# Kernel tuning notes

Hardware: AMD Instinct MI355X
Metric: run time of the kernel (lower is better)

## Reference

```python
import jax, jax.numpy as jnp
import numpy as np

B, S, H, D, R = 2, 2048, 16, 128, 16
HID = H * D
ROPE_BASE = 10000.0


def _rotate_half(x):
    x1, x2 = x[..., : D // 2], x[..., D // 2:]
    return jnp.concatenate((-x2, x1), axis=-1)


def _sin_cos(position_ids):
    # full-dim RoPE (rope_fraction == 1)
    inv_freq = 1.0 / (ROPE_BASE ** (jnp.arange(0, D, 2, dtype=jnp.float32) / D))  # [D/2]
    freqs = position_ids.astype(jnp.float32)[..., None] * inv_freq  # [B,S,D/2]
    emb = jnp.concatenate((freqs, freqs), axis=-1)  # [B,S,D]
    # add head axis -> [B,1,S,D]
    return jnp.sin(emb)[:, None], jnp.cos(emb)[:, None]


def setup_inputs() -> dict:
    key = jax.random.key(0)
    ks = jax.random.split(key, 6)
    q = jax.random.normal(ks[0], (B, S, HID), dtype=jnp.float32)
    k = jax.random.normal(ks[1], (B, S, HID), dtype=jnp.float32)
    v = jax.random.normal(ks[2], (B, S, HID), dtype=jnp.float32)
    position_ids = jnp.tile(jnp.arange(S, dtype=jnp.int64)[None], (B, 1))
    causal = jnp.tril(jnp.ones((S, S), dtype=bool))
    attention_mask = jnp.where(causal, 0.0, -1e9).astype(jnp.float32)
    attention_mask = jnp.broadcast_to(attention_mask[None, None], (B, 1, S, S))
    k_registers = jax.random.normal(ks[3], (1, H, R, D), dtype=jnp.float32)
    v_registers = jax.random.normal(ks[4], (1, H, R, D), dtype=jnp.float32)
    return {
        "query_states": q,
        "key_states": k,
        "value_states": v,
        "position_ids": position_ids,
        "attention_mask": attention_mask,
        "k_registers": k_registers,
        "v_registers": v_registers,
    }


def reference(query_states, key_states, value_states, position_ids,
              attention_mask, k_registers, v_registers):
    bsz, q_len, _ = query_states.shape
    # [B,S,H*D] -> [B,H,S,D]
    q = query_states.reshape(bsz, q_len, H, D).transpose(0, 2, 1, 3)
    k = key_states.reshape(bsz, -1, H, D).transpose(0, 2, 1, 3)
    v = value_states.reshape(bsz, -1, H, D).transpose(0, 2, 1, 3)

    sin, cos = _sin_cos(position_ids)
    q = q * cos + _rotate_half(q) * sin
    k = k * cos + _rotate_half(k) * sin

    # concat learned register K/V tokens along kv-length
    k = jnp.concatenate((k, jnp.broadcast_to(k_registers, (bsz, H, R, D))), axis=2)
    v = jnp.concatenate((v, jnp.broadcast_to(v_registers, (bsz, H, R, D))), axis=2)
    mask = jnp.concatenate(
        (attention_mask,
         jnp.zeros(attention_mask.shape[:-1] + (R,), dtype=attention_mask.dtype)),
        axis=-1)

    scale = 1.0 / np.sqrt(D).astype(np.float32)
    scores = jnp.einsum('bhqd,bhkd->bhqk', q, k * scale) + mask  # [B,H,S,S+R]
    probs = jax.nn.softmax(scores.astype(jnp.float32), axis=-1).astype(q.dtype)
    out = jnp.einsum('bhqk,bhkd->bhqd', probs, v)
    return out.transpose(0, 2, 1, 3).reshape(bsz, q_len, H * D)
```

## Files before the change

### kernel.cpp

```cpp
#include <hip/hip_runtime.h>

#define S_LEN 2048
#define HID   2048
#define NH    16
#define HD    128
#define NREG  16
#define KPAD  2112
#define NBH   32

typedef float f32x4 __attribute__((ext_vector_type(4)));
typedef short s16x8 __attribute__((ext_vector_type(8)));

__device__ __forceinline__ unsigned short f2bf(float f) {
    union { float f; unsigned int u; } x; x.f = f;
    return (unsigned short)((x.u + 0x7FFFu + ((x.u >> 16) & 1u)) >> 16);
}
__device__ __forceinline__ unsigned short f2bf_t(float f) {
    union { float f; unsigned int u; } x; x.f = f;
    return (unsigned short)(x.u >> 16);
}
__device__ __forceinline__ void gl_lds16(const unsigned short* g, unsigned short* l) {
    __builtin_amdgcn_global_load_lds((const __attribute__((address_space(1))) void*)g,
                                     (__attribute__((address_space(3))) void*)l, 16, 0, 0);
}
__device__ __forceinline__ void barrier_lgkm() {
    asm volatile("s_waitcnt lgkmcnt(0)\n\ts_barrier" ::: "memory");
}

__global__ void prepass_kernel(const float* __restrict__ k, const float* __restrict__ v,
                               const int* __restrict__ pos,
                               const float* __restrict__ kreg, const float* __restrict__ vreg,
                               unsigned short* __restrict__ Kb, unsigned short* __restrict__ Vt) {
    __shared__ unsigned short T[64][136];
    int bid = blockIdx.x, tid = threadIdx.x;

    if (bid < 4096) {
        int i  = bid * 256 + tid;
        int d4 = (i & 15) << 2;
        int h  = (i >> 4) & 15;
        int s  = (i >> 8) & 2047;
        int b  = i >> 19;
        float p = (float)pos[b * S_LEN + s];
        const float* kp = k + (size_t)(b * S_LEN + s) * HID + h * HD + d4;
        float4 k1 = *(const float4*)kp, k2 = *(const float4*)(kp + 64);
        const float* k1f = (const float*)&k1; const float* k2f = (const float*)&k2;
        unsigned short ok1[4], ok2[4];
        #pragma unroll
        for (int j = 0; j < 4; ++j) {
            float inv = exp2f((float)(d4 + j) * -0.20762050593046014f);
            float rev = p * inv * 0.15915494309189535f;
            rev -= rintf(rev);
            float a2 = rev * 6.283185307179586f;
            float sn = __sinf(a2), cs = __cosf(a2);
            ok1[j] = f2bf(k1f[j] * cs - k2f[j] * sn);
            ok2[j] = f2bf(k2f[j] * cs + k1f[j] * sn);
        }
        uint2 a;
        size_t ko = (size_t)((b * NH + h) * KPAD + s) * HD + d4;
        a.x = (unsigned)ok1[0] | ((unsigned)ok1[1] << 16);
        a.y = (unsigned)ok1[2] | ((unsigned)ok1[3] << 16);
        *(uint2*)(Kb + ko) = a;
        a.x = (unsigned)ok2[0] | ((unsigned)ok2[1] << 16);
        a.y = (unsigned)ok2[2] | ((unsigned)ok2[3] << 16);
        *(uint2*)(Kb + ko + 64) = a;
    } else if (bid < 5120) {
        int vb = bid - 4096;
        int tt = tid;
        int bh = vb >> 5, st = vb & 31;
        int b  = bh >> 4, h = bh & 15;
        {
            int key = tt >> 2, c = tt & 3;
            const float* src = v + (size_t)(b * S_LEN + st * 64 + key) * HID + h * HD;
            #pragma unroll
            for (int i = 0; i < 4; ++i) {
                int d0 = c * 32 + i * 8;
                float4 aa = *(const float4*)(src + d0);
                float4 bb = *(const float4*)(src + d0 + 4);
                unsigned short tmp[8] = { f2bf(aa.x), f2bf(aa.y), f2bf(aa.z), f2bf(aa.w),
                                          f2bf(bb.x), f2bf(bb.y), f2bf(bb.z), f2bf(bb.w) };
                *(uint4*)(&T[key][d0]) = *(const uint4*)tmp;
            }
        }
        __syncthreads();
        {
            int d = tt >> 1, half = tt & 1;
            unsigned short buf[32];
            #pragma unroll
            for (int i = 0; i < 32; ++i) buf[i] = T[half * 32 + i][d];
            uint4* dst = (uint4*)(Vt + ((size_t)(bh * HD + d)) * KPAD + st * 64 + half * 32);
            const uint4* bp = (const uint4*)buf;
            #pragma unroll
            for (int i = 0; i < 4; ++i) dst[i] = bp[i];
        }
    } else {
        int i = (bid - 5120) * 256 + tid;
        {
            int d = i & 127, r = (i >> 7) & 63, h = (i >> 13) & 15, b = i >> 17;
            float x = (r < NREG) ? kreg[(h * NREG + r) * HD + d] : 0.0f;
            Kb[((size_t)((b * NH + h) * KPAD + 2048 + r)) * HD + d] = f2bf(x);
        }
        {
            int r = i & 63, d = (i >> 6) & 127, h = (i >> 13) & 15, b = i >> 17;
            float x = (r < NREG) ? vreg[(h * NREG + r) * HD + d] : 0.0f;
            Vt[((size_t)((b * NH + h) * HD + d)) * KPAD + 2048 + r] = f2bf(x);
        }
    }
}

__global__ __launch_bounds__(256, 2)
void attn_kernel(const float* __restrict__ q, const int* __restrict__ pos,
                 const unsigned short* __restrict__ Kb,
                 const unsigned short* __restrict__ Vt, float* __restrict__ out) {
    __shared__ unsigned short Klds[64 * 128];
    __shared__ unsigned short Vtl[2 * 128 * 64];
    __shared__ unsigned short Plds[4 * 16 * 72];

    int idx = blockIdx.x;
    int bh  = idx & 31;
    int j5  = idx >> 5;
    int t   = (idx < 256) ? (15 - 2 * j5) : (2 * (j5 - 8));
    int b = bh >> 4, h = bh & 15;
    int tid = threadIdx.x, w = tid >> 6, lane = tid & 63;
    int quad = lane >> 4, k15 = lane & 15;
    int s0q = t * 128;

    const unsigned short* kg[4]; unsigned short* klp[4];
    const unsigned short* vg[4]; unsigned short* vlp[4];
    {
        int krow = 16 * w + (lane >> 4);
        #pragma unroll
        for (int j = 0; j < 4; ++j) {
            int key = krow + 4 * j;
            kg[j]  = Kb + ((size_t)bh * KPAD + key) * HD + (((lane & 15) ^ (key & 15)) << 3);
            klp[j] = Klds + (16 * w + 4 * j) * HD;
        }
        int drow = 32 * w + (lane >> 3);
        int vsw  = ((lane & 7) ^ (lane >> 3)) << 3;
        #pragma unroll
        for (int j = 0; j < 4; ++j) {
            vg[j]  = Vt + ((size_t)bh * HD + drow + 8 * j) * KPAD + vsw;
            vlp[j] = Vtl + (32 * w + 8 * j) * 64;
        }
    }
    auto stageK = [&](int kbase) {
        size_t ko = (size_t)kbase * HD;
        #pragma unroll
        for (int j = 0; j < 4; ++j) gl_lds16(kg[j] + ko, klp[j]);
    };
    auto stageV = [&](int kbase, int buf) {
        #pragma unroll
        for (int j = 0; j < 4; ++j) gl_lds16(vg[j] + kbase, vlp[j] + buf * 8192);
    };

    s16x8 qa[2][4];
    #pragma unroll
    for (int mt = 0; mt < 2; ++mt) {
        int row = s0q + w * 32 + mt * 16 + k15;
        float p = (float)pos[b * S_LEN + row];
        const float* qp = q + (size_t)(b * S_LEN + row) * HID + h * HD + quad * 8;
        #pragma unroll
        for (int kc = 0; kc < 2; ++kc) {
            float4 xa = *(const float4*)(qp + kc * 32);
            float4 xb = *(const float4*)(qp + kc * 32 + 4);
            float4 ya = *(const float4*)(qp + kc * 32 + 64);
            float4 yb = *(const float4*)(qp + kc * 32 + 68);
            float x1[8] = {xa.x, xa.y, xa.z, xa.w, xb.x, xb.y, xb.z, xb.w};
            float x2[8] = {ya.x, ya.y, ya.z, ya.w, yb.x, yb.y, yb.z, yb.w};
            unsigned short lo[8], hi[8];
            #pragma unroll
            for (int j = 0; j < 8; ++j) {
                int dh = kc * 32 + quad * 8 + j;
                float inv = exp2f((float)dh * -0.20762050593046014f);
                float rev = p * inv * 0.15915494309189535f;
                rev -= rintf(rev);
                float a2 = rev * 6.283185307179586f;
                float sn = __sinf(a2), cs = __cosf(a2);
                const float scale = 0.08838834764831845f;
                lo[j] = f2bf((x1[j] * cs - x2[j] * sn) * scale);
                hi[j] = f2bf((x2[j] * cs + x1[j] * sn) * scale);
            }
            qa[mt][kc]     = *(const s16x8*)lo;
            qa[mt][kc + 2] = *(const s16x8*)hi;
        }
    }

    f32x4 oacc[2][8];
    float lsum[2][4];
    #pragma unroll
    for (int mt = 0; mt < 2; ++mt) {
        #pragma unroll
        for (int nc = 0; nc < 8; ++nc) oacc[mt][nc] = (f32x4){0.f, 0.f, 0.f, 0.f};
        #pragma unroll
        for (int r = 0; r < 4; ++r) lsum[mt][r] = 0.f;
    }

    auto qk = [&](f32x4* sc, int mt, int mode) {
        #pragma unroll
        for (int nc = 0; nc < 4; ++nc) {
            sc[nc] = (f32x4){0.f, 0.f, 0.f, 0.f};
            if (mode == 2 && nc > 0) continue;
            #pragma unroll
            for (int kc = 0; kc < 4; ++kc) {
                const s16x8 bf = *(const s16x8*)(Klds + (nc * 16 + k15) * HD +
                                                 (((4 * kc + quad) ^ k15) << 3));
                sc[nc] = __builtin_amdgcn_mfma_f32_16x16x32_bf16(qa[mt][kc], bf, sc[nc], 0, 0, 0);
            }
        }
    };
    auto smax = [&](const f32x4* sc, int mt, int mode, int coff) {
        int rowb = w * 32 + mt * 16 + quad * 4;
        #pragma unroll
        for (int r = 0; r < 4; ++r) {
            float p[4];
            #pragma unroll
            for (int nc = 0; nc < 4; ++nc) {
                if (mode == 2 && nc > 0) { p[nc] = 0.f; continue; }
                float e = __expf(sc[nc][r]);
                bool valid = (mode != 1) || (coff + nc * 16 + k15 <= rowb + r);
                p[nc] = valid ? e : 0.f;
            }
            lsum[mt][r] += (p[0] + p[1]) + (p[2] + p[3]);
            int prow = w * (16 * 72) + (quad * 4 + r) * 72 + k15;
            Plds[prow]      = f2bf_t(p[0]);
            Plds[prow + 16] = f2bf_t(p[1]);
            Plds[prow + 32] = f2bf_t(p[2]);
            Plds[prow + 48] = f2bf_t(p[3]);
        }
    };
    auto pv = [&](int mt, int mode, const unsigned short* Vc) {
        #pragma unroll
        for (int kc = 0; kc < 2; ++kc) {
            if (mode == 2 && kc > 0) continue;
            const s16x8 pf = *(const s16x8*)(Plds + w * (16 * 72) + k15 * 72 +
                                             kc * 32 + quad * 8);
            #pragma unroll
            for (int nc = 0; nc < 8; ++nc) {
                const s16x8 vf = *(const s16x8*)(Vc + (nc * 16 + k15) * 64 +
                                                 (((4 * kc + quad) ^ (k15 & 7)) << 3));
                oacc[mt][nc] = __builtin_amdgcn_mfma_f32_16x16x32_bf16(pf, vf, oacc[mt][nc], 0, 0, 0);
            }
        }
    };

    stageK(0);
    stageV(0, 0);
    __syncthreads();

    int cur = 0;
    int NT  = 2 * t + 3;
    #pragma unroll 1
    for (int kt = 0; kt < NT; ++kt) {
        int  mode = (kt < 2 * t) ? 0 : ((kt < 2 * t + 2) ? 1 : 2);
        int  coff = 64 * (kt - 2 * t);
        bool more = (kt + 1 < NT);
        int  nkb  = (kt + 1 < 2 * t + 2) ? (kt + 1) * 64 : 2048;

        if (more) stageV(nkb, cur ^ 1);

        f32x4 sc[4];
        qk(sc, 0, mode);
        smax(sc, 0, mode, coff);
        qk(sc, 1, mode);

        barrier_lgkm();
        if (more) stageK(nkb);

        const unsigned short* Vc = Vtl + cur * 8192;
        pv(0, mode, Vc);
        smax(sc, 1, mode, coff);
        pv(1, mode, Vc);

        __syncthreads();
        cur ^= 1;
    }

    #pragma unroll
    for (int mt = 0; mt < 2; ++mt)
        #pragma unroll
        for (int r = 0; r < 4; ++r) {
            float lv = lsum[mt][r];
            #pragma unroll
            for (int off = 1; off < 16; off <<= 1) lv += __shfl_xor(lv, off);
            float invl = 1.0f / lv;
            size_t row = (size_t)(b * S_LEN + s0q + w * 32 + mt * 16 + quad * 4 + r) * HID
                         + h * HD + k15;
            #pragma unroll
            for (int nc = 0; nc < 8; ++nc)
                out[row + nc * 16] = oacc[mt][nc][r] * invl;
        }
}

extern "C" void kernel_launch(void* const* d_in, const int* in_sizes, int n_in,
                              void* d_out, int out_size, void* d_ws, size_t ws_size,
                              hipStream_t stream) {
    const float* q    = (const float*)d_in[0];
    const float* k    = (const float*)d_in[1];
    const float* v    = (const float*)d_in[2];
    const int*   pos  = (const int*)d_in[3];
    const float* kreg = (const float*)d_in[5];
    const float* vreg = (const float*)d_in[6];
    float* out = (float*)d_out;

    unsigned short* Kb = (unsigned short*)d_ws;
    unsigned short* Vt = Kb + (size_t)NBH * KPAD * HD;

    prepass_kernel<<<dim3(6144), dim3(256), 0, stream>>>(k, v, pos, kreg, vreg, Kb, Vt);
    attn_kernel<<<dim3(512), dim3(256), 0, stream>>>(q, pos, Kb, Vt, out);
}
```

Before: 243.9 us.

## Halve query tile to 64 rows, drop double-buffered V staging, launch more blocks

Each block now handles 64 query rows, one 16-row tile per wave, instead of 128, so twice as many blocks are launched and occupancy is raised to 3 blocks per CU. The double-buffered V LDS and the overlapped K/V staging are replaced by a simple stage-sync-compute loop. Blocks are ordered from the longest causal row block to the shortest. In exchange, each K/V tile is reused by half as many queries, and load latency is no longer hidden behind compute except through extra occupancy.

After: 211.3 us. 1.15x faster.

```diff
diff --git a/kernel.cpp b/kernel.cpp
--- a/kernel.cpp
+++ b/kernel.cpp
@@ -22,9 +22,6 @@
 __device__ __forceinline__ void gl_lds16(const unsigned short* g, unsigned short* l) {
     __builtin_amdgcn_global_load_lds((const __attribute__((address_space(1))) void*)g,
                                      (__attribute__((address_space(3))) void*)l, 16, 0, 0);
-}
-__device__ __forceinline__ void barrier_lgkm() {
-    asm volatile("s_waitcnt lgkmcnt(0)\n\ts_barrier" ::: "memory");
 }
 
 __global__ void prepass_kernel(const float* __restrict__ k, const float* __restrict__ v,
@@ -107,22 +104,21 @@
     }
 }
 
-__global__ __launch_bounds__(256, 2)
+__global__ __launch_bounds__(256, 3)
 void attn_kernel(const float* __restrict__ q, const int* __restrict__ pos,
                  const unsigned short* __restrict__ Kb,
                  const unsigned short* __restrict__ Vt, float* __restrict__ out) {
     __shared__ unsigned short Klds[64 * 128];
-    __shared__ unsigned short Vtl[2 * 128 * 64];
+    __shared__ unsigned short Vtl[128 * 64];
     __shared__ unsigned short Plds[4 * 16 * 72];
 
     int idx = blockIdx.x;
     int bh  = idx & 31;
-    int j5  = idx >> 5;
-    int t   = (idx < 256) ? (15 - 2 * j5) : (2 * (j5 - 8));
+    int m   = 31 - (idx >> 5);
     int b = bh >> 4, h = bh & 15;
     int tid = threadIdx.x, w = tid >> 6, lane = tid & 63;
     int quad = lane >> 4, k15 = lane & 15;
-    int s0q = t * 128;
+    int s0q = m * 64;
 
     const unsigned short* kg[4]; unsigned short* klp[4];
     const unsigned short* vg[4]; unsigned short* vlp[4];
@@ -142,20 +138,10 @@
             vlp[j] = Vtl + (32 * w + 8 * j) * 64;
         }
     }
-    auto stageK = [&](int kbase) {
-        size_t ko = (size_t)kbase * HD;
-        #pragma unroll
-        for (int j = 0; j < 4; ++j) gl_lds16(kg[j] + ko, klp[j]);
-    };
-    auto stageV = [&](int kbase, int buf) {
-        #pragma unroll
-        for (int j = 0; j < 4; ++j) gl_lds16(vg[j] + kbase, vlp[j] + buf * 8192);
-    };
-
-    s16x8 qa[2][4];
-    #pragma unroll
-    for (int mt = 0; mt < 2; ++mt) {
-        int row = s0q + w * 32 + mt * 16 + k15;
+
+    s16x8 qa[4];
+    {
+        int row = s0q + w * 16 + k15;
         float p = (float)pos[b * S_LEN + row];
         const float* qp = q + (size_t)(b * S_LEN + row) * HID + h * HD + quad * 8;
         #pragma unroll
@@ -179,22 +165,28 @@
                 lo[j] = f2bf((x1[j] * cs - x2[j] * sn) * scale);
                 hi[j] = f2bf((x2[j] * cs + x1[j] * sn) * scale);
             }
-            qa[mt][kc]     = *(const s16x8*)lo;
-            qa[mt][kc + 2] = *(const s16x8*)hi;
-        }
-    }
-
-    f32x4 oacc[2][8];
-    float lsum[2][4];
+            qa[kc]     = *(const s16x8*)lo;
+            qa[kc + 2] = *(const s16x8*)hi;
+        }
+    }
+
+    f32x4 oacc[8];
+    float lsum[4];
     #pragma unroll
-    for (int mt = 0; mt < 2; ++mt) {
-        #pragma unroll
-        for (int nc = 0; nc < 8; ++nc) oacc[mt][nc] = (f32x4){0.f, 0.f, 0.f, 0.f};
-        #pragma unroll
-        for (int r = 0; r < 4; ++r) lsum[mt][r] = 0.f;
-    }
-
-    auto qk = [&](f32x4* sc, int mt, int mode) {
+    for (int nc = 0; nc < 8; ++nc) oacc[nc] = (f32x4){0.f, 0.f, 0.f, 0.f};
+    #pragma unroll
+    for (int r = 0; r < 4; ++r) lsum[r] = 0.f;
+
+    auto stage = [&](int kbase) {
+        size_t ko = (size_t)kbase * HD;
+        #pragma unroll
+        for (int j = 0; j < 4; ++j) gl_lds16(kg[j] + ko, klp[j]);
+        #pragma unroll
+        for (int j = 0; j < 4; ++j) gl_lds16(vg[j] + kbase, vlp[j]);
+    };
+
+    auto tile = [&](int mode) {
+        f32x4 sc[4];
         #pragma unroll
         for (int nc = 0; nc < 4; ++nc) {
             sc[nc] = (f32x4){0.f, 0.f, 0.f, 0.f};
@@ -203,12 +195,10 @@
             for (int kc = 0; kc < 4; ++kc) {
                 const s16x8 bf = *(const s16x8*)(Klds + (nc * 16 + k15) * HD +
                                                  (((4 * kc + quad) ^ k15) << 3));
-                sc[nc] = __builtin_amdgcn_mfma_f32_16x16x32_bf16(qa[mt][kc], bf, sc[nc], 0, 0, 0);
-            }
-        }
-    };
-    auto smax = [&](const f32x4* sc, int mt, int mode, int coff) {
-        int rowb = w * 32 + mt * 16 + quad * 4;
+                sc[nc] = __builtin_amdgcn_mfma_f32_16x16x32_bf16(qa[kc], bf, sc[nc], 0, 0, 0);
+            }
+        }
+        int rowb = w * 16 + quad * 4;
         #pragma unroll
         for (int r = 0; r < 4; ++r) {
             float p[4];
@@ -216,18 +206,16 @@
             for (int nc = 0; nc < 4; ++nc) {
                 if (mode == 2 && nc > 0) { p[nc] = 0.f; continue; }
                 float e = __expf(sc[nc][r]);
-                bool valid = (mode != 1) || (coff + nc * 16 + k15 <= rowb + r);
+                bool valid = (mode != 1) || (nc * 16 + k15 <= rowb + r);
                 p[nc] = valid ? e : 0.f;
             }
-            lsum[mt][r] += (p[0] + p[1]) + (p[2] + p[3]);
+            lsum[r] += (p[0] + p[1]) + (p[2] + p[3]);
             int prow = w * (16 * 72) + (quad * 4 + r) * 72 + k15;
             Plds[prow]      = f2bf_t(p[0]);
             Plds[prow + 16] = f2bf_t(p[1]);
             Plds[prow + 32] = f2bf_t(p[2]);
             Plds[prow + 48] = f2bf_t(p[3]);
         }
-    };
-    auto pv = [&](int mt, int mode, const unsigned short* Vc) {
         #pragma unroll
         for (int kc = 0; kc < 2; ++kc) {
             if (mode == 2 && kc > 0) continue;
@@ -235,59 +223,40 @@
                                              kc * 32 + quad * 8);
             #pragma unroll
             for (int nc = 0; nc < 8; ++nc) {
-                const s16x8 vf = *(const s16x8*)(Vc + (nc * 16 + k15) * 64 +
+                const s16x8 vf = *(const s16x8*)(Vtl + (nc * 16 + k15) * 64 +
                                                  (((4 * kc + quad) ^ (k15 & 7)) << 3));
-                oacc[mt][nc] = __builtin_amdgcn_mfma_f32_16x16x32_bf16(pf, vf, oacc[mt][nc], 0, 0, 0);
+                oacc[nc] = __builtin_amdgcn_mfma_f32_16x16x32_bf16(pf, vf, oacc[nc], 0, 0, 0);
             }
         }
     };
 
-    stageK(0);
-    stageV(0, 0);
-    __syncthreads();
-
-    int cur = 0;
-    int NT  = 2 * t + 3;
-    #pragma unroll 1
-    for (int kt = 0; kt < NT; ++kt) {
-        int  mode = (kt < 2 * t) ? 0 : ((kt < 2 * t + 2) ? 1 : 2);
-        int  coff = 64 * (kt - 2 * t);
-        bool more = (kt + 1 < NT);
-        int  nkb  = (kt + 1 < 2 * t + 2) ? (kt + 1) * 64 : 2048;
-
-        if (more) stageV(nkb, cur ^ 1);
-
-        f32x4 sc[4];
-        qk(sc, 0, mode);
-        smax(sc, 0, mode, coff);
-        qk(sc, 1, mode);
-
-        barrier_lgkm();
-        if (more) stageK(nkb);
-
-        const unsigned short* Vc = Vtl + cur * 8192;
-        pv(0, mode, Vc);
-        smax(sc, 1, mode, coff);
-        pv(1, mode, Vc);
-
+    for (int kt = 0; kt < m; ++kt) {
         __syncthreads();
-        cur ^= 1;
-    }
+        stage(kt * 64);
+        __syncthreads();
+        tile(0);
+    }
+    __syncthreads();
+    stage(m * 64);
+    __syncthreads();
+    tile(1);
+    __syncthreads();
+    stage(2048);
+    __syncthreads();
+    tile(2);
 
     #pragma unroll
-    for (int mt = 0; mt < 2; ++mt)
-        #pragma unroll
-        for (int r = 0; r < 4; ++r) {
-            float lv = lsum[mt][r];
-            #pragma unroll
-            for (int off = 1; off < 16; off <<= 1) lv += __shfl_xor(lv, off);
-            float invl = 1.0f / lv;
-            size_t row = (size_t)(b * S_LEN + s0q + w * 32 + mt * 16 + quad * 4 + r) * HID
-                         + h * HD + k15;
-            #pragma unroll
-            for (int nc = 0; nc < 8; ++nc)
-                out[row + nc * 16] = oacc[mt][nc][r] * invl;
-        }
+    for (int r = 0; r < 4; ++r) {
+        float lv = lsum[r];
+        #pragma unroll
+        for (int off = 1; off < 16; off <<= 1) lv += __shfl_xor(lv, off);
+        float invl = 1.0f / lv;
+        size_t row = (size_t)(b * S_LEN + s0q + w * 16 + quad * 4 + r) * HID
+                     + h * HD + k15;
+        #pragma unroll
+        for (int nc = 0; nc < 8; ++nc)
+            out[row + nc * 16] = oacc[nc][r] * invl;
+    }
 }
 
 extern "C" void kernel_launch(void* const* d_in, const int* in_sizes, int n_in,
@@ -305,5 +274,5 @@
     unsigned short* Vt = Kb + (size_t)NBH * KPAD * HD;
 
     prepass_kernel<<<dim3(6144), dim3(256), 0, stream>>>(k, v, pos, kreg, vreg, Kb, Vt);
-    attn_kernel<<<dim3(512), dim3(256), 0, stream>>>(q, pos, Kb, Vt, out);
-}
+    attn_kernel<<<dim3(1024), dim3(256), 0, stream>>>(q, pos, Kb, Vt, out);
+}
```
